# Kernel tuning notes

Hardware: AMD Instinct MI355X
Metric: run time of the kernel (lower is better)

The kernel has to match this reference:

```python
import jax, jax.numpy as jnp
import numpy as np

# RecursiveNN: leaves -> embedding lookup; internal node -> sum of two children.
# For a binary tree, the root value equals the sum of all leaf embeddings,
# so the batched faithful form is gather + reduce over the leaf axis.

VOCAB = 100000
DIM = 300
B = 4096   # number of trees (sentences)
L = 64     # leaves per tree


def setup_inputs() -> dict:
    key = jax.random.key(0)
    k1, k2 = jax.random.split(key)
    word_ids = jax.random.randint(k1, (B, L), 0, VOCAB, dtype=jnp.int64 if jax.config.jax_enable_x64 else jnp.int32)
    embedding = jax.random.normal(k2, (VOCAB, DIM), dtype=jnp.float32)
    return {"word_ids": word_ids, "embedding": embedding}


def reference(word_ids, embedding):
    # [B, L, D] gather of leaf embeddings, then child-sum reduction to the root: [B, D]
    leaf_emb = embedding[word_ids]
    return leaf_emb.sum(axis=1)
```

## Files before the change

kernel.cpp:

```cpp
#include <hip/hip_runtime.h>


#define NB 4096
#define NL 64
#define ND 300
#define ND4 75

__global__ __launch_bounds__(256, 8) void recnn_root_sum(
    const int* __restrict__ word_ids,
    const float4* __restrict__ emb4,
    float* __restrict__ out)
{
    __shared__ float partial[4][ND];

    const int tid  = threadIdx.x;
    const int wave = tid >> 6;
    const int lane = tid & 63;

    const int tree_local = wave >> 1;
    const int half       = wave & 1;
    const int tree       = blockIdx.x * 2 + tree_local;

    const int myid = word_ids[tree * NL + half * 32 + (lane & 31)];

    float4 acc0 = make_float4(0.f, 0.f, 0.f, 0.f);

    #pragma unroll 8
    for (int i = 0; i < 32; ++i) {
        const int row = __builtin_amdgcn_readlane(myid, i);
        const float4 v = emb4[(size_t)row * ND4 + lane];
        acc0.x += v.x; acc0.y += v.y; acc0.z += v.z; acc0.w += v.w;
    }
    *reinterpret_cast<float4*>(&partial[wave][lane * 4]) = acc0;

    if (lane < ND4 - 64) {
        float4 acc1 = make_float4(0.f, 0.f, 0.f, 0.f);
        #pragma unroll 8
        for (int i = 0; i < 32; ++i) {
            const int row = __builtin_amdgcn_readlane(myid, i);
            const float4 v = emb4[(size_t)row * ND4 + 64 + lane];
            acc1.x += v.x; acc1.y += v.y; acc1.z += v.z; acc1.w += v.w;
        }
        *reinterpret_cast<float4*>(&partial[wave][256 + lane * 4]) = acc1;
    }
    __syncthreads();

    for (int t = tid; t < 2 * ND; t += 256) {
        const int tl = t / ND;
        const int c  = t - tl * ND;
        out[(size_t)(blockIdx.x * 2 + tl) * ND + c] =
            partial[2 * tl][c] + partial[2 * tl + 1][c];
    }
}

extern "C" void kernel_launch(void* const* d_in, const int* in_sizes, int n_in,
                              void* d_out, int out_size, void* d_ws, size_t ws_size,
                              hipStream_t stream) {
    const int*    word_ids = (const int*)d_in[0];
    const float4* emb4     = (const float4*)d_in[1];
    float*        out      = (float*)d_out;

    recnn_root_sum<<<NB / 2, 256, 0, stream>>>(word_ids, emb4, out);
}
```

Measured before the change: 195.2 us.

## Repack two embedding rows per wave iteration to fill all lanes

Each 75-float4 embedding row was previously gathered as a full 64-lane pass plus a second pass in which only 11 lanes were active. The new loop handles two rows per step and splits their 150 float4 across three loads (64, 64 and 22 lanes), so few lanes sit idle and more loads are in flight. Partial sums go into three shared arrays and are recombined by column ranges in the final reduction. The cost is more complex indexing, a divergent select on the second load, and a less regular reduction epilogue.

```diff
diff --git a/kernel.cpp b/kernel.cpp
--- a/kernel.cpp
+++ b/kernel.cpp
@@ -11,7 +11,9 @@
     const float4* __restrict__ emb4,
     float* __restrict__ out)
 {
-    __shared__ float partial[4][ND];
+    __shared__ float sA[4][64 * 4];
+    __shared__ float sB[4][64 * 4];
+    __shared__ float sC[4][22 * 4];
 
     const int tid  = threadIdx.x;
     const int wave = tid >> 6;
@@ -23,33 +25,59 @@
 
     const int myid = word_ids[tree * NL + half * 32 + (lane & 31)];
 
-    float4 acc0 = make_float4(0.f, 0.f, 0.f, 0.f);
+    const bool blo = lane < 11;
+    const bool cac = lane < 22;
 
-    #pragma unroll 8
-    for (int i = 0; i < 32; ++i) {
-        const int row = __builtin_amdgcn_readlane(myid, i);
-        const float4 v = emb4[(size_t)row * ND4 + lane];
-        acc0.x += v.x; acc0.y += v.y; acc0.z += v.z; acc0.w += v.w;
+    float4 accA = make_float4(0.f, 0.f, 0.f, 0.f);
+    float4 accB = make_float4(0.f, 0.f, 0.f, 0.f);
+    float4 accC = make_float4(0.f, 0.f, 0.f, 0.f);
+
+    #pragma unroll 1
+    for (int k = 0; k < 16; k += 2) {
+        float4 v[6];
+        #pragma unroll
+        for (int p = 0; p < 2; ++p) {
+            const int r0 = __builtin_amdgcn_readlane(myid, 2 * (k + p));
+            const int r1 = __builtin_amdgcn_readlane(myid, 2 * (k + p) + 1);
+            const size_t b0 = (size_t)r0 * ND4;
+            const size_t b1 = (size_t)r1 * ND4;
+            v[3 * p + 0] = emb4[b0 + lane];
+            v[3 * p + 1] = emb4[blo ? (b0 + 64 + lane) : (b1 + lane - 11)];
+            v[3 * p + 2] = cac ? emb4[b1 + 53 + lane]
+                               : make_float4(0.f, 0.f, 0.f, 0.f);
+        }
+        #pragma unroll
+        for (int p = 0; p < 2; ++p) {
+            accA.x += v[3*p+0].x; accA.y += v[3*p+0].y;
+            accA.z += v[3*p+0].z; accA.w += v[3*p+0].w;
+            accB.x += v[3*p+1].x; accB.y += v[3*p+1].y;
+            accB.z += v[3*p+1].z; accB.w += v[3*p+1].w;
+            accC.x += v[3*p+2].x; accC.y += v[3*p+2].y;
+            accC.z += v[3*p+2].z; accC.w += v[3*p+2].w;
+        }
     }
-    *reinterpret_cast<float4*>(&partial[wave][lane * 4]) = acc0;
 
-    if (lane < ND4 - 64) {
-        float4 acc1 = make_float4(0.f, 0.f, 0.f, 0.f);
-        #pragma unroll 8
-        for (int i = 0; i < 32; ++i) {
-            const int row = __builtin_amdgcn_readlane(myid, i);
-            const float4 v = emb4[(size_t)row * ND4 + 64 + lane];
-            acc1.x += v.x; acc1.y += v.y; acc1.z += v.z; acc1.w += v.w;
-        }
-        *reinterpret_cast<float4*>(&partial[wave][256 + lane * 4]) = acc1;
-    }
+    *reinterpret_cast<float4*>(&sA[wave][lane * 4]) = accA;
+    *reinterpret_cast<float4*>(&sB[wave][lane * 4]) = accB;
+    if (cac)
+        *reinterpret_cast<float4*>(&sC[wave][lane * 4]) = accC;
     __syncthreads();
 
-    for (int t = tid; t < 2 * ND; t += 256) {
-        const int tl = t / ND;
-        const int c  = t - tl * ND;
-        out[(size_t)(blockIdx.x * 2 + tl) * ND + c] =
-            partial[2 * tl][c] + partial[2 * tl + 1][c];
+    for (int x = tid; x < 2 * ND; x += 256) {
+        const int tl = x / ND;
+        const int c  = x - tl * ND;
+        const int c4 = c >> 2, j = c & 3;
+        float s = 0.f;
+        #pragma unroll
+        for (int wv = 0; wv < 2; ++wv) {
+            const int w = 2 * tl + wv;
+            float p;
+            if (c4 < 53)       p = sA[w][c4 * 4 + j] + sB[w][(c4 + 11) * 4 + j];
+            else if (c4 < 64)  p = sA[w][c4 * 4 + j] + sC[w][(c4 - 53) * 4 + j];
+            else               p = sB[w][(c4 - 64) * 4 + j] + sC[w][(c4 - 53) * 4 + j];
+            s += p;
+        }
+        out[(size_t)(blockIdx.x * 2 + tl) * ND + c] = s;
     }
 }
 
```

Result: no change. 192.5 us (-1.4%).
